# Performance work log

Measured on AMD Instinct MI355X. Metric: run time of the kernel, lower is better.

The kernel has to match this reference:

```python
import jax, jax.numpy as jnp
import numpy as np
import math

B, T, S, D, H = 2, 1024, 1024, 1024, 16
DH = D // H


def setup_inputs() -> dict:
    key = jax.random.key(0)
    ks = jax.random.split(key, 13)
    scale = 1.0 / math.sqrt(D)
    inp = {
        "q": jax.random.normal(ks[0], (B, T, D), jnp.float32),
        "k": jax.random.normal(ks[1], (B, S, D), jnp.float32),
        "v": jax.random.normal(ks[2], (B, S, D), jnp.float32),
        # causal mask: True means masked
        "attn_mask": jnp.broadcast_to(
            jnp.triu(jnp.ones((T, S), jnp.bool_), k=1)[None, None], (B, 1, T, S)
        ),
        "attn_bias": jax.random.normal(ks[3], (B, H, T, S), jnp.float32),
        "Wq": jax.random.normal(ks[4], (D, D), jnp.float32) * scale,
        "bq": jnp.zeros((D,), jnp.float32),
        "Wk": jax.random.normal(ks[5], (D, D), jnp.float32) * scale,
        "bk": jnp.zeros((D,), jnp.float32),
        "Wv": jax.random.normal(ks[6], (D, D), jnp.float32) * scale,
        "bv": jnp.zeros((D,), jnp.float32),
        "Wo": jax.random.normal(ks[7], (D, D), jnp.float32) * scale,
        "bo": jnp.zeros((D,), jnp.float32),
        "bias_scale": jnp.asarray(0.5, jnp.float32),
    }
    return inp


def reference(q, k, v, attn_mask, attn_bias, Wq, bq, Wk, bk, Wv, bv, Wo, bo, bias_scale):
    # projections (torch Linear convention: x @ W.T + b), split heads
    qh = (q @ Wq.T + bq).reshape(B, T, H, DH)   # (B,T,H,DH)
    kh = (k @ Wk.T + bk).reshape(B, S, H, DH)
    vh = (v @ Wv.T + bv).reshape(B, S, H, DH)

    scores = jnp.einsum("bthd,bshd->bhts", qh, kh) / math.sqrt(DH)  # (B,H,T,S)
    scores = jnp.clip(scores, -80.0, 80.0)
    scores = jnp.where(attn_mask, -jnp.inf, scores)  # mask broadcasts over H
    attn = jax.nn.softmax(scores, axis=-1)

    # post-softmax multiplicative bias + renormalize
    scale = 1.0 + bias_scale * jnp.tanh(attn_bias)
    attn = attn * jnp.maximum(scale, 1e-9)
    attn = attn / (jnp.sum(attn, axis=-1, keepdims=True) + 1e-9)

    # dropout p=0.0 (eval) -> identity
    out = jnp.einsum("bhts,bshd->bthd", attn, vh).reshape(B, T, D)
    out = out @ Wo.T + bo
    return out, attn
```

## Files before the change

kernel.cpp:

```cpp
#include <hip/hip_runtime.h>
#include <hip/hip_bf16.h>
#include <math.h>

#define BB 2
#define TT 1024
#define SS 1024
#define DD 1024
#define HH 16
#define DH 64

typedef __attribute__((ext_vector_type(8))) short bf16x8;
typedef __attribute__((ext_vector_type(4))) float f32x4;
typedef unsigned short ushort_t;

#define AS3(p) ((__attribute__((address_space(3))) unsigned int*)(p))
#define AS1(p) ((const __attribute__((address_space(1))) unsigned int*)(p))

__device__ __forceinline__ unsigned short f2b(float f) {
    union { float f; unsigned u; } x; x.f = f;
    unsigned r = x.u + 0x7FFFu + ((x.u >> 16) & 1u);
    return (unsigned short)(r >> 16);
}

__device__ __forceinline__ bf16x8 pack_bf16x8(float4 a, float4 b) {
    union { unsigned u[4]; bf16x8 v; } r;
    asm("v_cvt_pk_bf16_f32 %0, %1, %2" : "=v"(r.u[0]) : "v"(a.x), "v"(a.y));
    asm("v_cvt_pk_bf16_f32 %0, %1, %2" : "=v"(r.u[1]) : "v"(a.z), "v"(a.w));
    asm("v_cvt_pk_bf16_f32 %0, %1, %2" : "=v"(r.u[2]) : "v"(b.x), "v"(b.y));
    asm("v_cvt_pk_bf16_f32 %0, %1, %2" : "=v"(r.u[3]) : "v"(b.z), "v"(b.w));
    return r.v;
}

__global__ __launch_bounds__(256) void cvt_all(
    const float* __restrict__ q, const float* __restrict__ k, const float* __restrict__ v,
    const float* __restrict__ Wq, const float* __restrict__ Wk,
    const float* __restrict__ Wv, const float* __restrict__ Wo,
    ushort_t* __restrict__ oq, ushort_t* __restrict__ ok, ushort_t* __restrict__ ov,
    ushort_t* __restrict__ oWq, ushort_t* __restrict__ oWk,
    ushort_t* __restrict__ oWv, ushort_t* __restrict__ oWo)
{
    const int y = blockIdx.y;
    if (y >= 3 && blockIdx.x >= 512) return;
    const float* src =
        (y == 0) ? q : (y == 1) ? k : (y == 2) ? v :
        (y == 3) ? Wq : (y == 4) ? Wk : (y == 5) ? Wv : Wo;
    ushort_t* dst =
        (y == 0) ? oq : (y == 1) ? ok : (y == 2) ? ov :
        (y == 3) ? oWq : (y == 4) ? oWk : (y == 5) ? oWv : oWo;
    size_t i = ((size_t)blockIdx.x * 256 + threadIdx.x) * 8;
    float4 v0 = *(const float4*)&src[i];
    float4 v1 = *(const float4*)&src[i + 4];
    uint4 o;
    o.x = f2b(v0.x) | ((unsigned)f2b(v0.y) << 16);
    o.y = f2b(v0.z) | ((unsigned)f2b(v0.w) << 16);
    o.z = f2b(v1.x) | ((unsigned)f2b(v1.y) << 16);
    o.w = f2b(v1.z) | ((unsigned)f2b(v1.w) << 16);
    *(uint4*)&dst[i] = o;
}

__device__ __forceinline__ void gemm128_mainloop(
    const ushort_t* __restrict__ A,
    const ushort_t* __restrict__ Bw,
    int K, ushort_t (*Asm)[128 * 32], ushort_t (*Bsm)[128 * 32],
    f32x4 acc[4][4])
{
    const int tid = threadIdx.x;
    const int wave = tid >> 6, lane = tid & 63;
    const int sr = lane >> 2;
    const int gc = (lane & 3) ^ ((lane >> 3) & 3);
    const int l15 = lane & 15, q = lane >> 4;
    const int mblk = (wave >> 1) * 64, nblk = (wave & 1) * 64;

#define G128_STAGE(k0_, b_) do {                                               \
        _Pragma("unroll")                                                      \
        for (int o = 0; o < 2; o++) {                                          \
            int r0 = (wave * 2 + o) * 16;                                      \
            __builtin_amdgcn_global_load_lds(                                  \
                AS1(A + (size_t)(r0 + sr) * K + (k0_) + gc * 8),               \
                AS3(Asm[b_] + r0 * 32), 16, 0, 0);                             \
            __builtin_amdgcn_global_load_lds(                                  \
                AS1(Bw + (size_t)(r0 + sr) * K + (k0_) + gc * 8),              \
                AS3(Bsm[b_] + r0 * 32), 16, 0, 0);                             \
        } } while (0)

#define G128_COMPUTE(b_) do {                                                  \
        bf16x8 av[4], bv[4];                                                   \
        _Pragma("unroll")                                                      \
        for (int mi = 0; mi < 4; mi++) {                                       \
            int r = mblk + mi * 16 + l15;                                      \
            av[mi] = *(const bf16x8*)&Asm[b_][r * 32 + (q ^ ((r >> 1) & 3)) * 8]; \
        }                                                                      \
        _Pragma("unroll")                                                      \
        for (int ni = 0; ni < 4; ni++) {                                       \
            int r = nblk + ni * 16 + l15;                                      \
            bv[ni] = *(const bf16x8*)&Bsm[b_][r * 32 + (q ^ ((r >> 1) & 3)) * 8]; \
        }                                                                      \
        _Pragma("unroll")                                                      \
        for (int mi = 0; mi < 4; mi++)                                         \
            _Pragma("unroll")                                                  \
            for (int ni = 0; ni < 4; ni++)                                     \
                acc[mi][ni] = __builtin_amdgcn_mfma_f32_16x16x32_bf16(         \
                    av[mi], bv[ni], acc[mi][ni], 0, 0, 0);                     \
        } while (0)

    G128_STAGE(0, 0);
    __syncthreads();

    int buf = 0;
    for (int k0 = 0; k0 < K; k0 += 32) {
        if (k0 + 32 < K) G128_STAGE(k0 + 32, buf ^ 1);
        G128_COMPUTE(buf);
        __syncthreads();
        buf ^= 1;
    }
#undef G128_STAGE
#undef G128_COMPUTE
}

__global__ __launch_bounds__(256) void proj_gemm(
    const ushort_t* __restrict__ qb, const ushort_t* __restrict__ kb, const ushort_t* __restrict__ vb,
    const ushort_t* __restrict__ Wqb, const ushort_t* __restrict__ Wkb, const ushort_t* __restrict__ Wvb,
    const float* __restrict__ bq, const float* __restrict__ bk, const float* __restrict__ bv,
    ushort_t* __restrict__ qh, ushort_t* __restrict__ kh, ushort_t* __restrict__ vh)
{
    __shared__ ushort_t Asm[2][128 * 32];
    __shared__ ushort_t Bsm[2][128 * 32];
    const int z = blockIdx.z;
    const ushort_t* A = (z == 0) ? qb : (z == 1) ? kb : vb;
    const ushort_t* W = (z == 0) ? Wqb : (z == 1) ? Wkb : Wvb;
    const float* bias = (z == 0) ? bq : (z == 1) ? bk : bv;
    ushort_t* Y = (z == 0) ? qh : (z == 1) ? kh : vh;

    const int bm = blockIdx.y * 128, bn = blockIdx.x * 128;
    f32x4 acc[4][4];
    #pragma unroll
    for (int i = 0; i < 4; i++)
        #pragma unroll
        for (int j = 0; j < 4; j++) acc[i][j] = (f32x4)(0.f);

    gemm128_mainloop(A + (size_t)bm * DD, W + (size_t)bn * DD, DD, Asm, Bsm, acc);

    const int lane = threadIdx.x & 63, wave = threadIdx.x >> 6;
    const int mblk = (wave >> 1) * 64, nblk = (wave & 1) * 64;
    const int l15 = lane & 15, q = lane >> 4;
    #pragma unroll
    for (int mi = 0; mi < 4; mi++) {
        #pragma unroll
        for (int ni = 0; ni < 4; ni++) {
            int col = bn + nblk + ni * 16 + l15;
            float bcol = bias[col];
            #pragma unroll
            for (int r = 0; r < 4; r++) {
                int row = bm + mblk + mi * 16 + q * 4 + r;
                Y[(size_t)row * DD + col] = f2b(acc[mi][ni][r] + bcol);
            }
        }
    }
}

__global__ __launch_bounds__(256) void oproj_gemm(
    const ushort_t* __restrict__ A, const ushort_t* __restrict__ W,
    const float* __restrict__ bias, float* __restrict__ Y)
{
    __shared__ ushort_t Asm[2][128 * 32];
    __shared__ ushort_t Bsm[2][128 * 32];
    const int bm = blockIdx.y * 128, bn = blockIdx.x * 128;
    f32x4 acc[4][4];
    #pragma unroll
    for (int i = 0; i < 4; i++)
        #pragma unroll
        for (int j = 0; j < 4; j++) acc[i][j] = (f32x4)(0.f);

    gemm128_mainloop(A + (size_t)bm * DD, W + (size_t)bn * DD, DD, Asm, Bsm, acc);

    const int lane = threadIdx.x & 63, wave = threadIdx.x >> 6;
    const int mblk = (wave >> 1) * 64, nblk = (wave & 1) * 64;
    const int l15 = lane & 15, q = lane >> 4;
    #pragma unroll
    for (int mi = 0; mi < 4; mi++) {
        #pragma unroll
        for (int ni = 0; ni < 4; ni++) {
            int col = bn + nblk + ni * 16 + l15;
            float bcol = bias[col];
            #pragma unroll
            for (int r = 0; r < 4; r++) {
                int row = bm + mblk + mi * 16 + q * 4 + r;
                Y[(size_t)row * DD + col] = acc[mi][ni][r] + bcol;
            }
        }
    }
}

__global__ __launch_bounds__(256) void transpose_v(
    const ushort_t* __restrict__ vh, ushort_t* __restrict__ vT)
{
    __shared__ ushort_t Ls[64][72];
    const int s0 = blockIdx.x * 64;
    const int bh = blockIdx.y;
    const int b = bh >> 4, h = bh & 15;
    const int tid = threadIdx.x;
    const int r = tid >> 2, c16 = (tid & 3) * 16;

    const ushort_t* src = &vh[((size_t)(b * SS + s0 + r) * HH + h) * DH + c16];
    uint4 u0 = *(const uint4*)src;
    uint4 u1 = *(const uint4*)(src + 8);
    ushort_t tmp[16];
    *(uint4*)&tmp[0] = u0; *(uint4*)&tmp[8] = u1;
    #pragma unroll
    for (int j = 0; j < 16; j++) Ls[c16 + j][r] = tmp[j];
    __syncthreads();

    const int dh = r;
    uint4 w0 = *(const uint4*)&Ls[dh][c16];
    uint4 w1 = *(const uint4*)&Ls[dh][c16 + 8];
    ushort_t* dst = &vT[((size_t)bh * DH + dh) * SS + s0 + c16];
    *(uint4*)dst = w0;
    *(uint4*)(dst + 8) = w1;
}

__global__ __launch_bounds__(256) void scores_sm_mfma(
    const ushort_t* __restrict__ qh, const ushort_t* __restrict__ kh,
    const float* __restrict__ attn_bias, const float* __restrict__ bias_scale_p,
    float* __restrict__ wout, float* __restrict__ Ppart, float* __restrict__ Wpart)
{
    __shared__ ushort_t Qs[128 * 64];
    __shared__ ushort_t Ks[128 * 64];
    __shared__ float pPs[128][2];
    __shared__ float pWs[128][2];

    int idx = blockIdx.x, ti = 0;
    while (idx >= ti + 1) { idx -= ti + 1; ti++; }
    const int si = idx;
    const int bh = blockIdx.y;
    const int b = bh >> 4, h = bh & 15;
    const int t0 = ti * 128, s0 = si * 128;

    const int tid = threadIdx.x;
    const int wave = tid >> 6, lane = tid & 63;
    const int sr8 = lane >> 3;
    const int gc8 = (lane & 7) ^ sr8;

    #pragma unroll
    for (int o = 0; o < 4; o++) {
        int r0 = (wave * 4 + o) * 8;
        int r = r0 + sr8;
        __builtin_amdgcn_global_load_lds(
            AS1(qh + ((size_t)(b * TT + t0 + r) * HH + h) * DH + gc8 * 8),
            AS3(Qs + r0 * 64), 16, 0, 0);
        __builtin_amdgcn_global_load_lds(
            AS1(kh + ((size_t)(b * SS + s0 + r) * HH + h) * DH + gc8 * 8),
            AS3(Ks + r0 * 64), 16, 0, 0);
    }
    __syncthreads();

    const int l15 = lane & 15, q = lane >> 4;
    const int tblk = (wave >> 1) * 64, sblk = (wave & 1) * 64;
    f32x4 acc[4][4];
    #pragma unroll
    for (int i = 0; i < 4; i++)
        #pragma unroll
        for (int j = 0; j < 4; j++) acc[i][j] = (f32x4)(0.f);

    #pragma unroll
    for (int ks = 0; ks < 2; ks++) {
        bf16x8 av[4], bv[4];
        #pragma unroll
        for (int mi = 0; mi < 4; mi++) {
            int r = tblk + mi * 16 + l15;
            av[mi] = *(const bf16x8*)&Qs[r * 64 + ((ks * 4 + q) ^ (r & 7)) * 8];
        }
        #pragma unroll
        for (int ni = 0; ni < 4; ni++) {
            int r = sblk + ni * 16 + l15;
            bv[ni] = *(const bf16x8*)&Ks[r * 64 + ((ks * 4 + q) ^ (r & 7)) * 8];
        }
        #pragma unroll
        for (int mi = 0; mi < 4; mi++)
            #pragma unroll
            for (int ni = 0; ni < 4; ni++)
                acc[mi][ni] = __builtin_amdgcn_mfma_f32_16x16x32_bf16(av[mi], bv[ni], acc[mi][ni], 0, 0, 0);
    }

    const float bscale = bias_scale_p[0];
    float rowP[4][4], rowW[4][4];
    #pragma unroll
    for (int mi = 0; mi < 4; mi++)
        #pragma unroll
        for (int r = 0; r < 4; r++) { rowP[mi][r] = 0.f; rowW[mi][r] = 0.f; }

    #pragma unroll
    for (int mi = 0; mi < 4; mi++) {
        #pragma unroll
        for (int ni = 0; ni < 4; ni++) {
            int scol = s0 + sblk + ni * 16 + l15;
            #pragma unroll
            for (int r = 0; r < 4; r++) {
                int t = t0 + tblk + mi * 16 + q * 4 + r;
                float s = acc[mi][ni][r] * 0.125f;
                s = fminf(fmaxf(s, -80.f), 80.f);
                float p = (scol <= t) ? __expf(s - 16.f) : 0.f;
                float bvv = attn_bias[((size_t)bh * TT + t) * SS + scol];
                float e = __expf(-2.f * fabsf(bvv));
                float th = copysignf((1.f - e) / (1.f + e), bvv);
                float sc = fmaxf(1.f + bscale * th, 1e-9f);
                float w = p * sc;
                wout[((size_t)bh * TT + t) * SS + scol] = w;
                rowP[mi][r] += p;
                rowW[mi][r] += w;
            }
        }
    }

    #pragma unroll
    for (int off = 1; off < 16; off <<= 1) {
        #pragma unroll
        for (int mi = 0; mi < 4; mi++)
            #pragma unroll
            for (int r = 0; r < 4; r++) {
                rowP[mi][r] += __shfl_xor(rowP[mi][r], off);
                rowW[mi][r] += __shfl_xor(rowW[mi][r], off);
            }
    }
    if (l15 == 0) {
        #pragma unroll
        for (int mi = 0; mi < 4; mi++)
            #pragma unroll
            for (int r = 0; r < 4; r++) {
                int row = tblk + mi * 16 + q * 4 + r;
                pPs[row][wave & 1] = rowP[mi][r];
                pWs[row][wave & 1] = rowW[mi][r];
            }
    }
    __syncthreads();
    if (tid < 128) {
        float P2 = pPs[tid][0] + pPs[tid][1];
        float W2 = pWs[tid][0] + pWs[tid][1];
        size_t o = ((size_t)bh * TT + t0 + tid) * 8 + si;
        Ppart[o] = P2;
        Wpart[o] = W2;
    }
}

__global__ __launch_bounds__(256) void av_norm_mfma(
    const float* __restrict__ w, const ushort_t* __restrict__ vT,
    const float* __restrict__ Ppart, const float* __restrict__ Wpart,
    float* __restrict__ attn, ushort_t* __restrict__ ao)
{
    __shared__ ushort_t Vsm[2][64 * 64];
    __shared__ float Wsm[2][64 * 64];
    __shared__ float sInv[64];

    const int tb = (int)gridDim.x - 1 - (int)blockIdx.x;
    const int bh = blockIdx.y;
    const int b = bh >> 4, h = bh & 15;
    const int t0 = tb * 64;
    const int nst = tb + 1;

    const int tid = threadIdx.x;
    const int wave = tid >> 6, lane = tid & 63;
    const int sr8 = lane >> 3, gc8 = (lane & 7) ^ sr8;
    const int l15 = lane & 15, q = lane >> 4;

    if (tid < 64) {
        int t = t0 + tid;
        int n2 = (t >> 7) + 1;
        const float* pp = Ppart + ((size_t)bh * TT + t) * 8;
        const float* ww = Wpart + ((size_t)bh * TT + t) * 8;
        float P = 0.f, W = 0.f;
        for (int j = 0; j < n2; j++) { P += pp[j]; W += ww[j]; }
        sInv[tid] = 1.f / (W + 1e-9f * P);
    }

    float* aout_base = attn + ((size_t)bh * TT + t0) * SS;

    {
        float4 z = make_float4(0.f, 0.f, 0.f, 0.f);
        const int zr = tid >> 4, zc = (tid & 15) * 4;
        for (int si = nst; si < SS / 64; si++)
            #pragma unroll
            for (int kk = 0; kk < 4; kk++)
                *(float4*)&aout_base[(size_t)(zr + kk * 16) * SS + si * 64 + zc] = z;
    }

    const float* arow = w + ((size_t)bh * TT + t0 + wave * 16 + l15) * SS + q * 8;
    const ushort_t* vbase = vT + (size_t)bh * DH * SS;
    const float* wtile_base = w + ((size_t)bh * TT + t0) * SS;

    f32x4 acc[4];
    #pragma unroll
    for (int i = 0; i < 4; i++) acc[i] = (f32x4)(0.f);

#define STAGE_V(sidx, bb) do {                                                \
        _Pragma("unroll")                                                     \
        for (int o = 0; o < 2; o++) {                                         \
            int r0 = wave * 16 + o * 8;                                       \
            __builtin_amdgcn_global_load_lds(                                 \
                AS1(vbase + (size_t)(r0 + sr8) * SS + (sidx) * 64 + gc8 * 8), \
                AS3(&Vsm[bb][r0 * 64]), 16, 0, 0);                            \
        } } while (0)

#define STAGE_W(sidx, bb) do {                                                \
        _Pragma("unroll")                                                     \
        for (int i_ = 0; i_ < 4; i_++) {                                      \
            int row_ = wave * 16 + i_ * 4 + (lane >> 4);                      \
            __builtin_amdgcn_global_load_lds(                                 \
                AS1(wtile_base + (size_t)row_ * SS + (sidx) * 64 + (lane & 15) * 4), \
                AS3(&Wsm[bb][wave * 1024 + i_ * 256]), 16, 0, 0);             \
        } } while (0)

#define LOAD_A(sidx, dst) do {                                                \
        const float* p_ = arow + (sidx) * 64;                                 \
        dst[0] = *(const float4*)(p_);                                        \
        dst[1] = *(const float4*)(p_ + 4);                                    \
        dst[2] = *(const float4*)(p_ + 32);                                   \
        dst[3] = *(const float4*)(p_ + 36); } while (0)

#define COMPUTE(bb, ax) do {                                                  \
        bf16x8 af0 = pack_bf16x8(ax[0], ax[1]);                               \
        bf16x8 af1 = pack_bf16x8(ax[2], ax[3]);                               \
        _Pragma("unroll")                                                     \
        for (int ni = 0; ni < 4; ni++) {                                      \
            int rv = ni * 16 + l15;                                           \
            bf16x8 b0 = *(const bf16x8*)&Vsm[bb][rv * 64 + ((q) ^ (rv & 7)) * 8];       \
            bf16x8 b1 = *(const bf16x8*)&Vsm[bb][rv * 64 + ((4 + q) ^ (rv & 7)) * 8];   \
            acc[ni] = __builtin_amdgcn_mfma_f32_16x16x32_bf16(af0, b0, acc[ni], 0, 0, 0);\
            acc[ni] = __builtin_amdgcn_mfma_f32_16x16x32_bf16(af1, b1, acc[ni], 0, 0, 0);\
        } } while (0)

#define WRITEBACK(bb, sidx) do {                                              \
        const int wc_ = (tid & 15) * 4;                                       \
        _Pragma("unroll")                                                     \
        for (int kk = 0; kk < 4; kk++) {                                      \
            int row_ = (tid >> 4) + kk * 16;                                  \
            float4 vv = *(const float4*)&Wsm[bb][row_ * 64 + wc_];            \
            float iv_ = sInv[row_];                                           \
            vv.x *= iv_; vv.y *= iv_; vv.z *= iv_; vv.w *= iv_;               \
            *(float4*)&aout_base[(size_t)row_ * SS + (sidx) * 64 + wc_] = vv; \
        } } while (0)

    float4 aA[4], aB[4];
    STAGE_V(0, 0);
    STAGE_W(0, 0);
    LOAD_A(0, aA);
    __syncthreads();

    int st = 0;
    while (true) {
        if (st + 1 < nst) { STAGE_V(st + 1, 1); STAGE_W(st + 1, 1); LOAD_A(st + 1, aB); }
        COMPUTE(0, aA);
        WRITEBACK(0, st);
        __syncthreads();
        if (++st == nst) break;
        if (st + 1 < nst) { STAGE_V(st + 1, 0); STAGE_W(st + 1, 0); LOAD_A(st + 1, aA); }
        COMPUTE(1, aB);
        WRITEBACK(1, st);
        __syncthreads();
        if (++st == nst) break;
    }
#undef STAGE_V
#undef STAGE_W
#undef LOAD_A
#undef COMPUTE
#undef WRITEBACK

    #pragma unroll
    for (int ni = 0; ni < 4; ni++) {
        int dh = ni * 16 + l15;
        #pragma unroll
        for (int r = 0; r < 4; r++) {
            int trow = wave * 16 + q * 4 + r;
            float iv = sInv[trow];
            int t = t0 + trow;
            ao[(size_t)(b * TT + t) * DD + h * DH + dh] = f2b(acc[ni][r] * iv);
        }
    }
}

extern "C" void kernel_launch(void* const* d_in, const int* in_sizes, int n_in,
                              void* d_out, int out_size, void* d_ws, size_t ws_size,
                              hipStream_t stream)
{
    const float* q   = (const float*)d_in[0];
    const float* k   = (const float*)d_in[1];
    const float* v   = (const float*)d_in[2];
    const float* attn_bias = (const float*)d_in[4];
    const float* Wq = (const float*)d_in[5];
    const float* bq = (const float*)d_in[6];
    const float* Wk = (const float*)d_in[7];
    const float* bk = (const float*)d_in[8];
    const float* Wv = (const float*)d_in[9];
    const float* bv = (const float*)d_in[10];
    const float* Wo = (const float*)d_in[11];
    const float* bo = (const float*)d_in[12];
    const float* bscale = (const float*)d_in[13];

    char* base = (char*)d_ws;
    ushort_t* qb  = (ushort_t*)(base + (0ull << 20));
    ushort_t* kb  = (ushort_t*)(base + (4ull << 20));
    ushort_t* vb  = (ushort_t*)(base + (8ull << 20));
    ushort_t* Wqb = (ushort_t*)(base + (12ull << 20));
    ushort_t* Wkb = (ushort_t*)(base + (14ull << 20));
    ushort_t* Wvb = (ushort_t*)(base + (16ull << 20));
    ushort_t* Wob = (ushort_t*)(base + (18ull << 20));
    ushort_t* qhb = (ushort_t*)(base + (20ull << 20));
    ushort_t* khb = (ushort_t*)(base + (24ull << 20));
    ushort_t* vhb = (ushort_t*)(base + (28ull << 20));
    ushort_t* vT  = qb;
    ushort_t* aob = kb;
    float* PpartB = (float*)(base + (8ull << 20));
    float* WpartB = (float*)(base + (9ull << 20));

    float* out  = (float*)d_out;
    float* attn = out + (size_t)BB * TT * DD;

    cvt_all<<<dim3(1024, 7), 256, 0, stream>>>(q, k, v, Wq, Wk, Wv, Wo,
                                               qb, kb, vb, Wqb, Wkb, Wvb, Wob);
    proj_gemm<<<dim3(8, 16, 3), 256, 0, stream>>>(qb, kb, vb, Wqb, Wkb, Wvb,
                                                  bq, bk, bv, qhb, khb, vhb);
    transpose_v<<<dim3(16, 32), 256, 0, stream>>>(vhb, vT);
    scores_sm_mfma<<<dim3(36, 32), 256, 0, stream>>>(qhb, khb, attn_bias, bscale,
                                                     attn, PpartB, WpartB);
    av_norm_mfma<<<dim3(16, 32), 256, 0, stream>>>(attn, vT, PpartB, WpartB,
                                                   attn, aob);
    oproj_gemm<<<dim3(8, 16), 256, 0, stream>>>(aob, Wob, bo, out);
}
```

Before: 373.2 us.

## Fuse V transpose into projection epilogue, widen GEMM K-tile, stage bias via LDS

The V projection epilogue now writes the transposed head layout directly, so the separate transpose_v kernel and its extra round trip through global memory are removed. The shared GEMM mainloop doubles its K tile from 32 to 64 with an 8-way XOR swizzle, halving the number of barriers per output tile at the cost of twice the LDS. The scores kernel now brings the attn_bias tile into LDS with async global-to-LDS loads, part of it overlapped with the QK MFMA loop, and reuses the Q/K shared buffer to hold it. Risks include lower occupancy from the larger LDS footprint, extra barriers, and scattered 8-byte stores into vT.

```diff
diff --git a/kernel.cpp b/kernel.cpp
--- a/kernel.cpp
+++ b/kernel.cpp
@@ -61,54 +61,56 @@
 __device__ __forceinline__ void gemm128_mainloop(
     const ushort_t* __restrict__ A,
     const ushort_t* __restrict__ Bw,
-    int K, ushort_t (*Asm)[128 * 32], ushort_t (*Bsm)[128 * 32],
+    int K, ushort_t (*Asm)[128 * 64], ushort_t (*Bsm)[128 * 64],
     f32x4 acc[4][4])
 {
     const int tid = threadIdx.x;
     const int wave = tid >> 6, lane = tid & 63;
-    const int sr = lane >> 2;
-    const int gc = (lane & 3) ^ ((lane >> 3) & 3);
+    const int sr8 = lane >> 3;
+    const int gc8 = (lane & 7) ^ sr8;
     const int l15 = lane & 15, q = lane >> 4;
     const int mblk = (wave >> 1) * 64, nblk = (wave & 1) * 64;
 
 #define G128_STAGE(k0_, b_) do {                                               \
         _Pragma("unroll")                                                      \
-        for (int o = 0; o < 2; o++) {                                          \
-            int r0 = (wave * 2 + o) * 16;                                      \
+        for (int o = 0; o < 4; o++) {                                          \
+            int r0 = wave * 32 + o * 8;                                        \
             __builtin_amdgcn_global_load_lds(                                  \
-                AS1(A + (size_t)(r0 + sr) * K + (k0_) + gc * 8),               \
-                AS3(Asm[b_] + r0 * 32), 16, 0, 0);                             \
+                AS1(A + (size_t)(r0 + sr8) * K + (k0_) + gc8 * 8),             \
+                AS3(Asm[b_] + r0 * 64), 16, 0, 0);                             \
             __builtin_amdgcn_global_load_lds(                                  \
-                AS1(Bw + (size_t)(r0 + sr) * K + (k0_) + gc * 8),              \
-                AS3(Bsm[b_] + r0 * 32), 16, 0, 0);                             \
+                AS1(Bw + (size_t)(r0 + sr8) * K + (k0_) + gc8 * 8),            \
+                AS3(Bsm[b_] + r0 * 64), 16, 0, 0);                             \
         } } while (0)
 
 #define G128_COMPUTE(b_) do {                                                  \
-        bf16x8 av[4], bv[4];                                                   \
         _Pragma("unroll")                                                      \
-        for (int mi = 0; mi < 4; mi++) {                                       \
-            int r = mblk + mi * 16 + l15;                                      \
-            av[mi] = *(const bf16x8*)&Asm[b_][r * 32 + (q ^ ((r >> 1) & 3)) * 8]; \
-        }                                                                      \
-        _Pragma("unroll")                                                      \
-        for (int ni = 0; ni < 4; ni++) {                                       \
-            int r = nblk + ni * 16 + l15;                                      \
-            bv[ni] = *(const bf16x8*)&Bsm[b_][r * 32 + (q ^ ((r >> 1) & 3)) * 8]; \
-        }                                                                      \
-        _Pragma("unroll")                                                      \
-        for (int mi = 0; mi < 4; mi++)                                         \
+        for (int ks = 0; ks < 2; ks++) {                                       \
+            bf16x8 av[4], bv[4];                                               \
             _Pragma("unroll")                                                  \
-            for (int ni = 0; ni < 4; ni++)                                     \
-                acc[mi][ni] = __builtin_amdgcn_mfma_f32_16x16x32_bf16(         \
-                    av[mi], bv[ni], acc[mi][ni], 0, 0, 0);                     \
-        } while (0)
+            for (int mi = 0; mi < 4; mi++) {                                   \
+                int r = mblk + mi * 16 + l15;                                  \
+                av[mi] = *(const bf16x8*)&Asm[b_][r * 64 + ((ks * 4 + q) ^ (r & 7)) * 8]; \
+            }                                                                  \
+            _Pragma("unroll")                                                  \
+            for (int ni = 0; ni < 4; ni++) {                                   \
+                int r = nblk + ni * 16 + l15;                                  \
+                bv[ni] = *(const bf16x8*)&Bsm[b_][r * 64 + ((ks * 4 + q) ^ (r & 7)) * 8]; \
+            }                                                                  \
+            _Pragma("unroll")                                                  \
+            for (int mi = 0; mi < 4; mi++)                                     \
+                _Pragma("unroll")                                              \
+                for (int ni = 0; ni < 4; ni++)                                 \
+                    acc[mi][ni] = __builtin_amdgcn_mfma_f32_16x16x32_bf16(     \
+                        av[mi], bv[ni], acc[mi][ni], 0, 0, 0);                 \
+        } } while (0)
 
     G128_STAGE(0, 0);
     __syncthreads();
 
     int buf = 0;
-    for (int k0 = 0; k0 < K; k0 += 32) {
-        if (k0 + 32 < K) G128_STAGE(k0 + 32, buf ^ 1);
+    for (int k0 = 0; k0 < K; k0 += 64) {
+        if (k0 + 64 < K) G128_STAGE(k0 + 64, buf ^ 1);
         G128_COMPUTE(buf);
         __syncthreads();
         buf ^= 1;
@@ -121,15 +123,14 @@
     const ushort_t* __restrict__ qb, const ushort_t* __restrict__ kb, const ushort_t* __restrict__ vb,
     const ushort_t* __restrict__ Wqb, const ushort_t* __restrict__ Wkb, const ushort_t* __restrict__ Wvb,
     const float* __restrict__ bq, const float* __restrict__ bk, const float* __restrict__ bv,
-    ushort_t* __restrict__ qh, ushort_t* __restrict__ kh, ushort_t* __restrict__ vh)
-{
-    __shared__ ushort_t Asm[2][128 * 32];
-    __shared__ ushort_t Bsm[2][128 * 32];
+    ushort_t* __restrict__ qh, ushort_t* __restrict__ kh, ushort_t* __restrict__ vT)
+{
+    __shared__ ushort_t Asm[2][128 * 64];
+    __shared__ ushort_t Bsm[2][128 * 64];
     const int z = blockIdx.z;
     const ushort_t* A = (z == 0) ? qb : (z == 1) ? kb : vb;
     const ushort_t* W = (z == 0) ? Wqb : (z == 1) ? Wkb : Wvb;
     const float* bias = (z == 0) ? bq : (z == 1) ? bk : bv;
-    ushort_t* Y = (z == 0) ? qh : (z == 1) ? kh : vh;
 
     const int bm = blockIdx.y * 128, bn = blockIdx.x * 128;
     f32x4 acc[4][4];
@@ -143,16 +144,39 @@
     const int lane = threadIdx.x & 63, wave = threadIdx.x >> 6;
     const int mblk = (wave >> 1) * 64, nblk = (wave & 1) * 64;
     const int l15 = lane & 15, q = lane >> 4;
-    #pragma unroll
-    for (int mi = 0; mi < 4; mi++) {
-        #pragma unroll
-        for (int ni = 0; ni < 4; ni++) {
-            int col = bn + nblk + ni * 16 + l15;
-            float bcol = bias[col];
-            #pragma unroll
-            for (int r = 0; r < 4; r++) {
-                int row = bm + mblk + mi * 16 + q * 4 + r;
-                Y[(size_t)row * DD + col] = f2b(acc[mi][ni][r] + bcol);
+
+    if (z < 2) {
+        ushort_t* Y = (z == 0) ? qh : kh;
+        #pragma unroll
+        for (int mi = 0; mi < 4; mi++) {
+            #pragma unroll
+            for (int ni = 0; ni < 4; ni++) {
+                int col = bn + nblk + ni * 16 + l15;
+                float bcol = bias[col];
+                #pragma unroll
+                for (int r = 0; r < 4; r++) {
+                    int row = bm + mblk + mi * 16 + q * 4 + r;
+                    Y[(size_t)row * DD + col] = f2b(acc[mi][ni][r] + bcol);
+                }
+            }
+        }
+    } else {
+        #pragma unroll
+        for (int mi = 0; mi < 4; mi++) {
+            int row0 = bm + mblk + mi * 16 + q * 4;
+            int b_ = row0 >> 10, s0_ = row0 & 1023;
+            #pragma unroll
+            for (int ni = 0; ni < 4; ni++) {
+                int col = bn + nblk + ni * 16 + l15;
+                float bcol = bias[col];
+                int h_ = col >> 6, dh_ = col & 63;
+                union { unsigned u[2]; } pk;
+                pk.u[0] = (unsigned)f2b(acc[mi][ni][0] + bcol)
+                        | ((unsigned)f2b(acc[mi][ni][1] + bcol) << 16);
+                pk.u[1] = (unsigned)f2b(acc[mi][ni][2] + bcol)
+                        | ((unsigned)f2b(acc[mi][ni][3] + bcol) << 16);
+                *(uint2*)&vT[((size_t)(b_ * 16 + h_) * 64 + dh_) * SS + s0_] =
+                    make_uint2(pk.u[0], pk.u[1]);
             }
         }
     }
@@ -162,8 +186,8 @@
     const ushort_t* __restrict__ A, const ushort_t* __restrict__ W,
     const float* __restrict__ bias, float* __restrict__ Y)
 {
-    __shared__ ushort_t Asm[2][128 * 32];
-    __shared__ ushort_t Bsm[2][128 * 32];
+    __shared__ ushort_t Asm[2][128 * 64];
+    __shared__ ushort_t Bsm[2][128 * 64];
     const int bm = blockIdx.y * 128, bn = blockIdx.x * 128;
     f32x4 acc[4][4];
     #pragma unroll
@@ -191,40 +215,15 @@
     }
 }
 
-__global__ __launch_bounds__(256) void transpose_v(
-    const ushort_t* __restrict__ vh, ushort_t* __restrict__ vT)
-{
-    __shared__ ushort_t Ls[64][72];
-    const int s0 = blockIdx.x * 64;
-    const int bh = blockIdx.y;
-    const int b = bh >> 4, h = bh & 15;
-    const int tid = threadIdx.x;
-    const int r = tid >> 2, c16 = (tid & 3) * 16;
-
-    const ushort_t* src = &vh[((size_t)(b * SS + s0 + r) * HH + h) * DH + c16];
-    uint4 u0 = *(const uint4*)src;
-    uint4 u1 = *(const uint4*)(src + 8);
-    ushort_t tmp[16];
-    *(uint4*)&tmp[0] = u0; *(uint4*)&tmp[8] = u1;
-    #pragma unroll
-    for (int j = 0; j < 16; j++) Ls[c16 + j][r] = tmp[j];
-    __syncthreads();
-
-    const int dh = r;
-    uint4 w0 = *(const uint4*)&Ls[dh][c16];
-    uint4 w1 = *(const uint4*)&Ls[dh][c16 + 8];
-    ushort_t* dst = &vT[((size_t)bh * DH + dh) * SS + s0 + c16];
-    *(uint4*)dst = w0;
-    *(uint4*)(dst + 8) = w1;
-}
-
-__global__ __launch_bounds__(256) void scores_sm_mfma(
+__global__ __launch_bounds__(256) void scores_fused(
     const ushort_t* __restrict__ qh, const ushort_t* __restrict__ kh,
     const float* __restrict__ attn_bias, const float* __restrict__ bias_scale_p,
     float* __restrict__ wout, float* __restrict__ Ppart, float* __restrict__ Wpart)
 {
-    __shared__ ushort_t Qs[128 * 64];
-    __shared__ ushort_t Ks[128 * 64];
+    __shared__ ushort_t SMEM[32768];
+    ushort_t* Qs = SMEM;
+    ushort_t* Ks = SMEM + 8192;
+    float* BiasF = (float*)SMEM;
     __shared__ float pPs[128][2];
     __shared__ float pWs[128][2];
 
@@ -253,6 +252,15 @@
     }
     __syncthreads();
 
+    #pragma unroll
+    for (int o = 0; o < 8; o++) {
+        int tl = 64 + wave * 16 + o * 2;
+        __builtin_amdgcn_global_load_lds(
+            AS1(attn_bias + ((size_t)(bh * TT + t0 + tl + (lane >> 5)) * SS
+                             + s0 + (lane & 31) * 4)),
+            AS3(BiasF + tl * 128), 16, 0, 0);
+    }
+
     const int l15 = lane & 15, q = lane >> 4;
     const int tblk = (wave >> 1) * 64, sblk = (wave & 1) * 64;
     f32x4 acc[4][4];
@@ -280,6 +288,17 @@
             for (int ni = 0; ni < 4; ni++)
                 acc[mi][ni] = __builtin_amdgcn_mfma_f32_16x16x32_bf16(av[mi], bv[ni], acc[mi][ni], 0, 0, 0);
     }
+    __syncthreads();
+
+    #pragma unroll
+    for (int o = 0; o < 8; o++) {
+        int tl = wave * 16 + o * 2;
+        __builtin_amdgcn_global_load_lds(
+            AS1(attn_bias + ((size_t)(bh * TT + t0 + tl + (lane >> 5)) * SS
+                             + s0 + (lane & 31) * 4)),
+            AS3(BiasF + tl * 128), 16, 0, 0);
+    }
+    __syncthreads();
 
     const float bscale = bias_scale_p[0];
     float rowP[4][4], rowW[4][4];
@@ -292,14 +311,15 @@
     for (int mi = 0; mi < 4; mi++) {
         #pragma unroll
         for (int ni = 0; ni < 4; ni++) {
-            int scol = s0 + sblk + ni * 16 + l15;
+            int s_l = sblk + ni * 16 + l15;
+            int scol = s0 + s_l;
             #pragma unroll
             for (int r = 0; r < 4; r++) {
-                int t = t0 + tblk + mi * 16 + q * 4 + r;
-                float s = acc[mi][ni][r] * 0.125f;
-                s = fminf(fmaxf(s, -80.f), 80.f);
+                int t_l = tblk + mi * 16 + q * 4 + r;
+                int t = t0 + t_l;
+                float s = fminf(fmaxf(acc[mi][ni][r] * 0.125f, -80.f), 80.f);
                 float p = (scol <= t) ? __expf(s - 16.f) : 0.f;
-                float bvv = attn_bias[((size_t)bh * TT + t) * SS + scol];
+                float bvv = BiasF[t_l * 128 + s_l];
                 float e = __expf(-2.f * fabsf(bvv));
                 float th = copysignf((1.f - e) / (1.f + e), bvv);
                 float sc = fmaxf(1.f + bscale * th, 1e-9f);
@@ -504,8 +524,7 @@
     ushort_t* Wob = (ushort_t*)(base + (18ull << 20));
     ushort_t* qhb = (ushort_t*)(base + (20ull << 20));
     ushort_t* khb = (ushort_t*)(base + (24ull << 20));
-    ushort_t* vhb = (ushort_t*)(base + (28ull << 20));
-    ushort_t* vT  = qb;
+    ushort_t* vT  = (ushort_t*)(base + (28ull << 20));
     ushort_t* aob = kb;
     float* PpartB = (float*)(base + (8ull << 20));
     float* WpartB = (float*)(base + (9ull << 20));
@@ -516,10 +535,9 @@
     cvt_all<<<dim3(1024, 7), 256, 0, stream>>>(q, k, v, Wq, Wk, Wv, Wo,
                                                qb, kb, vb, Wqb, Wkb, Wvb, Wob);
     proj_gemm<<<dim3(8, 16, 3), 256, 0, stream>>>(qb, kb, vb, Wqb, Wkb, Wvb,
-                                                  bq, bk, bv, qhb, khb, vhb);
-    transpose_v<<<dim3(16, 32), 256, 0, stream>>>(vhb, vT);
-    scores_sm_mfma<<<dim3(36, 32), 256, 0, stream>>>(qhb, khb, attn_bias, bscale,
-                                                     attn, PpartB, WpartB);
+                                                  bq, bk, bv, qhb, khb, vT);
+    scores_fused<<<dim3(36, 32), 256, 0, stream>>>(qhb, khb, attn_bias, bscale,
+                                                   attn, PpartB, WpartB);
     av_norm_mfma<<<dim3(16, 32), 256, 0, stream>>>(attn, vT, PpartB, WpartB,
                                                    attn, aob);
     oproj_gemm<<<dim3(8, 16), 256, 0, stream>>>(aob, Wob, bo, out);
```

Measured after the change: 381.0 us. +2.1%, slower.
